# Kernel tuning notes

Measured on AMD Instinct MI355X. Metric: run time of the kernel, lower is better.

Reference implementation:

```python
import jax, jax.numpy as jnp
import numpy as np

B = 16384   # batch
D = 768     # in_features == out_features
H = 768     # expert_hidden_size (must equal D, see MoRALayer wiring)
E = 4       # num_experts_per_level
L = 2       # num_levels
K = 2       # SparseMoE top-k
T = 10      # max_act_steps
LN_EPS = 1e-5


def setup_inputs() -> dict:
    key = jax.random.key(0)
    ks = jax.random.split(key, 8)
    s = 0.02
    return {
        "x": jax.random.normal(ks[0], (B, D), jnp.float32),
        # LSTMCell params (torch gate order i,f,g,o)
        "Wi": jax.random.normal(ks[1], (4 * H, D), jnp.float32) * s,
        "Wh": jax.random.normal(ks[2], (4 * H, H), jnp.float32) * s,
        "bi": jnp.zeros((4 * H,), jnp.float32),
        "bh": jnp.zeros((4 * H,), jnp.float32),
        # halting head
        "Whalt": jax.random.normal(ks[3], (1, H), jnp.float32) * s,
        "bhalt": jnp.zeros((1,), jnp.float32),
        # hierarchical MoE params, stacked over levels (all dims equal: D==H)
        "gateW": jax.random.normal(ks[4], (L, E, H), jnp.float32) * s,
        "gateb": jnp.zeros((L, E), jnp.float32),
        "W1": jax.random.normal(ks[5], (L, E, H, H), jnp.float32) * s,
        "b1": jnp.zeros((L, E, H), jnp.float32),
        "W2": jax.random.normal(ks[6], (L, E, D, H), jnp.float32) * s,
        "b2": jnp.zeros((L, E, D), jnp.float32),
        # LayerNorm
        "gamma": jnp.ones((D,), jnp.float32),
        "beta": jnp.zeros((D,), jnp.float32),
    }


def _act(x, Wi, Wh, bi, bh, Whalt, bhalt):
    """AdaptiveComputationTime: fixed T LSTM steps (faithful worst-case of the
    data-dependent early break). Returns rem * mean_t(h_t) per the torch math:
    avg = sum_t(h_t * rem_final) / n_updates, with rem_final broadcast over t."""
    b = x.shape[0]
    h0 = jnp.zeros((b, H), x.dtype)
    c0 = jnp.zeros((b, H), x.dtype)
    hp0 = jnp.zeros((b, 1), x.dtype)
    rem0 = jnp.zeros((b, 1), x.dtype)
    hsum0 = jnp.zeros((b, H), x.dtype)
    xWi = x @ Wi.T + bi + bh  # constant across steps

    def step(carry, _):
        h, c, hp, rem, hsum = carry
        gates = xWi + h @ Wh.T
        i, f, g, o = jnp.split(gates, 4, axis=-1)
        c = jax.nn.sigmoid(f) * c + jax.nn.sigmoid(i) * jnp.tanh(g)
        h = jax.nn.sigmoid(o) * jnp.tanh(c)
        y = jax.nn.sigmoid(h @ Whalt.T + bhalt)  # [b,1]
        hp = hp + y * (1.0 - hp)
        rem = rem + 1.0 - hp
        return (h, c, hp, rem, hsum + h), None

    (h, c, hp, rem, hsum), _ = jax.lax.scan(
        step, (h0, c0, hp0, rem0, hsum0), None, length=T)
    n_updates = jnp.asarray(float(T), x.dtype)
    avg = rem * hsum / n_updates  # [b,H]
    return avg, hp, n_updates


def _sparse_moe(x, Wg, bg, W1, b1, W2, b2):
    """Top-k expert routing (intended semantics of the torch SparseMoE)."""
    logits = x @ Wg.T + bg                                   # [b,E]
    w, idx = jax.lax.top_k(logits, K)                        # [b,K]
    w = jax.nn.softmax(w, axis=-1)
    hmid = jax.nn.relu(jnp.einsum('bi,ehi->beh', x, W1) + b1)  # [b,E,H]
    eo = jnp.einsum('beh,eoh->beo', hmid, W2) + b2             # [b,E,D]
    sel = jnp.take_along_axis(eo, idx[:, :, None], axis=1)     # [b,K,D]
    return jnp.sum(w[:, :, None] * sel, axis=1)                # [b,D]


def reference(x, Wi, Wh, bi, bh, Whalt, bhalt,
              gateW, gateb, W1, b1, W2, b2, gamma, beta):
    h, _hp, _n = _act(x, Wi, Wh, bi, bh, Whalt, bhalt)
    for l in range(L):
        h = _sparse_moe(h, gateW[l], gateb[l], W1[l], b1[l], W2[l], b2[l])
    mu = jnp.mean(h, axis=-1, keepdims=True)
    var = jnp.mean(jnp.square(h - mu), axis=-1, keepdims=True)
    return (h - mu) * jax.lax.rsqrt(var + LN_EPS) * gamma + beta
```

## Files before the change

### kernel.cpp

```cpp
#include <hip/hip_runtime.h>
#include <cstdint>
#include <cstddef>

#define Bn 16384
#define Dn 768
#define Hn 768
#define G4 3072
#define Tn 10
#define LO_SCALE 4096.0f
#define LO_INV   (1.0f/4096.0f)

typedef _Float16 f16;
typedef _Float16 f16x8 __attribute__((ext_vector_type(8)));
typedef float    f32x4 __attribute__((ext_vector_type(4)));

__device__ __forceinline__ float sigm(float x) { return 1.f / (1.f + expf(-x)); }

__device__ __forceinline__ void gll16(const void* g, void* l) {
    __builtin_amdgcn_global_load_lds((const __attribute__((address_space(1))) void*)g,
                                     (__attribute__((address_space(3))) void*)l, 16, 0, 0);
}

template <bool SPLIT, int EPI, bool BIAS, bool RELU>
__global__ __launch_bounds__(256) void mgemm(
    const f16* __restrict__ Ah, const f16* __restrict__ Al, int lda,
    const f16* __restrict__ Bh, const f16* __restrict__ Bl,
    float* __restrict__ Cf, f16* __restrict__ Ch, f16* __restrict__ Cl, int ldc,
    const float* __restrict__ bias,
    const float* __restrict__ xwi, float* __restrict__ cst, float* __restrict__ hsum,
    f16* __restrict__ hh_out, f16* __restrict__ hl_out,
    long aZ, long bZ, long cZ, long biasZ)
{
    const int z = blockIdx.z;
    if (z) {
        Ah += (long)z * aZ; if (SPLIT) Al += (long)z * aZ;
        Bh += (long)z * bZ; if (SPLIT) Bl += (long)z * bZ;
        if (EPI == 0) Cf += (long)z * cZ;
        if (EPI == 1 || EPI == 2) { Ch += (long)z * cZ; if (EPI == 1) Cl += (long)z * cZ; }
        if (BIAS) bias += (long)z * biasZ;
    }
    __shared__ __align__(16) f16 sA[2][4096];
    __shared__ __align__(16) f16 sB[2][4096];

    const int tid  = threadIdx.x;
    const int w    = tid >> 6, lane = tid & 63;
    const int quad = lane >> 4, l15 = lane & 15;
    const int m0 = blockIdx.x * 128, n0 = blockIdx.y * 128;
    const int wm = (w >> 1) * 64,   wn = (w & 1) * 64;

    f32x4 acc[4][4], accx[4][4];
#pragma unroll
    for (int i = 0; i < 4; i++)
#pragma unroll
        for (int j = 0; j < 4; j++) {
            acc[i][j]  = (f32x4){0.f, 0.f, 0.f, 0.f};
            accx[i][j] = (f32x4){0.f, 0.f, 0.f, 0.f};
        }

    for (int k0 = 0; k0 < 768; k0 += 32) {
        __syncthreads();
#pragma unroll
        for (int u = 0; u < 2; u++) {
            int s = u * 256 + tid;
            int r = s >> 2;
            int c = ((s & 3) - (r >> 1)) & 3;
            gll16(Ah + (long)(m0 + r) * lda + k0 + c * 8, &sA[0][s * 8]);
            gll16(Bh + (long)(n0 + r) * 768 + k0 + c * 8, &sB[0][s * 8]);
            if (SPLIT) {
                gll16(Al + (long)(m0 + r) * lda + k0 + c * 8, &sA[1][s * 8]);
                gll16(Bl + (long)(n0 + r) * 768 + k0 + c * 8, &sB[1][s * 8]);
            }
        }
        __syncthreads();

        f16x8 ah[4], al[4], bh[4], bl[4];
#pragma unroll
        for (int t = 0; t < 4; t++) {
            int ra = wm + t * 16 + l15;
            int ca = (quad + (ra >> 1)) & 3;
            ah[t] = *(const f16x8*)&sA[0][ra * 32 + ca * 8];
            if (SPLIT) al[t] = *(const f16x8*)&sA[1][ra * 32 + ca * 8];
            int rb = wn + t * 16 + l15;
            int cb = (quad + (rb >> 1)) & 3;
            bh[t] = *(const f16x8*)&sB[0][rb * 32 + cb * 8];
            if (SPLIT) bl[t] = *(const f16x8*)&sB[1][rb * 32 + cb * 8];
        }
#pragma unroll
        for (int i = 0; i < 4; i++)
#pragma unroll
            for (int j = 0; j < 4; j++) {
                acc[i][j] = __builtin_amdgcn_mfma_f32_16x16x32_f16(ah[i], bh[j], acc[i][j], 0, 0, 0);
                if (SPLIT) {
                    accx[i][j] = __builtin_amdgcn_mfma_f32_16x16x32_f16(ah[i], bl[j], accx[i][j], 0, 0, 0);
                    accx[i][j] = __builtin_amdgcn_mfma_f32_16x16x32_f16(al[i], bh[j], accx[i][j], 0, 0, 0);
                }
            }
    }

    if (EPI == 3) {
        const int j = ((n0 + wn) >> 2) + l15;
#pragma unroll
        for (int i = 0; i < 4; i++) {
#pragma unroll
            for (int reg = 0; reg < 4; reg++) {
                int r = m0 + wm + i * 16 + quad * 4 + reg;
                long xb = (long)r * G4 + n0 + wn + l15;
                float iv = acc[i][0][reg] + accx[i][0][reg] * LO_INV + xwi[xb];
                float fv = acc[i][1][reg] + accx[i][1][reg] * LO_INV + xwi[xb + 16];
                float gv = acc[i][2][reg] + accx[i][2][reg] * LO_INV + xwi[xb + 32];
                float ov = acc[i][3][reg] + accx[i][3][reg] * LO_INV + xwi[xb + 48];
                long ci = (long)r * Hn + j;
                float cv = sigm(fv) * cst[ci] + sigm(iv) * tanhf(gv);
                float hv = sigm(ov) * tanhf(cv);
                cst[ci] = cv;
                hsum[ci] += hv;
                f16 hh = (f16)hv;
                hh_out[ci] = hh;
                hl_out[ci] = (f16)((hv - (float)hh) * LO_SCALE);
            }
        }
    } else {
#pragma unroll
        for (int i = 0; i < 4; i++)
#pragma unroll
            for (int j = 0; j < 4; j++) {
                int col = n0 + wn + j * 16 + l15;
                float bv = BIAS ? bias[col] : 0.f;
#pragma unroll
                for (int reg = 0; reg < 4; reg++) {
                    int r = m0 + wm + i * 16 + quad * 4 + reg;
                    float v = acc[i][j][reg] + (SPLIT ? accx[i][j][reg] * LO_INV : 0.f) + bv;
                    if (RELU) v = v > 0.f ? v : 0.f;
                    long o = (long)r * ldc + col;
                    if (EPI == 0) Cf[o] = v;
                    else if (EPI == 2) Ch[o] = (f16)v;
                    else {
                        f16 hh = (f16)v;
                        Ch[o] = hh;
                        Cl[o] = (f16)((v - (float)hh) * LO_SCALE);
                    }
                }
            }
    }
}


__global__ void split_plain_k(const float* __restrict__ src, f16* __restrict__ dh,
                              f16* __restrict__ dl, long n) {
    long i = (long)blockIdx.x * 256 + threadIdx.x;
    if (i < n) {
        float v = src[i];
        f16 h = (f16)v;
        dh[i] = h;
        dl[i] = (f16)((v - (float)h) * LO_SCALE);
    }
}

__global__ void split_perm_k(const float* __restrict__ src, f16* __restrict__ dh,
                             f16* __restrict__ dl) {
    int P = blockIdx.x;
    int q = ((P >> 4) & 3) * Hn + (P >> 6) * 16 + (P & 15);
    const float* s = src + (long)q * 768;
    long o = (long)P * 768;
#pragma unroll
    for (int u = 0; u < 3; u++) {
        int kk = threadIdx.x + u * 256;
        float v = s[kk];
        f16 h = (f16)v;
        dh[o + kk] = h;
        dl[o + kk] = (f16)((v - (float)h) * LO_SCALE);
    }
}

__global__ void bsum_perm_k(const float* __restrict__ bi, const float* __restrict__ bh,
                            float* __restrict__ bsum) {
    int P = blockIdx.x * 256 + threadIdx.x;
    if (P < G4) {
        int q = ((P >> 4) & 3) * Hn + (P >> 6) * 16 + (P & 15);
        bsum[P] = bi[q] + bh[q];
    }
}

__global__ __launch_bounds__(256) void lstm0_k(
    const float* __restrict__ xwi, float* __restrict__ cst, float* __restrict__ hsum,
    f16* __restrict__ hh, f16* __restrict__ hl,
    float* __restrict__ hp, float* __restrict__ rem,
    const float* __restrict__ Whalt, const float* __restrict__ bhalt)
{
    const int row = blockIdx.x, tid = threadIdx.x;
    const float* xr = xwi + (long)row * G4;
    const long hb = (long)row * Hn;
    float part = 0.f;
#pragma unroll
    for (int u = 0; u < 3; u++) {
        int j = tid + u * 256;
        int Pb = (j >> 4) * 64 + (j & 15);
        float iv = xr[Pb], fv = xr[Pb + 16], gv = xr[Pb + 32], ov = xr[Pb + 48];
        (void)fv;
        float cv = sigm(iv) * tanhf(gv);
        float hv = sigm(ov) * tanhf(cv);
        cst[hb + j] = cv;
        hsum[hb + j] = hv;
        f16 h = (f16)hv;
        hh[hb + j] = h;
        hl[hb + j] = (f16)((hv - (float)h) * LO_SCALE);
        part += hv * Whalt[j];
    }
    __shared__ float red[256];
    red[tid] = part;
    __syncthreads();
    for (int s = 128; s > 0; s >>= 1) {
        if (tid < s) red[tid] += red[tid + s];
        __syncthreads();
    }
    if (tid == 0) {
        float y = sigm(red[0] + bhalt[0]);
        hp[row] = y;
        rem[row] = 1.f - y;
    }
}

__global__ __launch_bounds__(256) void halt_k(
    const f16* __restrict__ hh, const f16* __restrict__ hl,
    float* __restrict__ hp, float* __restrict__ rem,
    const float* __restrict__ Whalt, const float* __restrict__ bhalt)
{
    const int row = blockIdx.x, tid = threadIdx.x;
    const long hb = (long)row * Hn;
    float part = 0.f;
#pragma unroll
    for (int u = 0; u < 3; u++) {
        int j = tid + u * 256;
        float hv = (float)hh[hb + j] + (float)hl[hb + j] * LO_INV;
        part += hv * Whalt[j];
    }
    __shared__ float red[256];
    red[tid] = part;
    __syncthreads();
    for (int s = 128; s > 0; s >>= 1) {
        if (tid < s) red[tid] += red[tid + s];
        __syncthreads();
    }
    if (tid == 0) {
        float y = sigm(red[0] + bhalt[0]);
        float p = hp[row];
        float np = p + y * (1.f - p);
        hp[row] = np;
        rem[row] += 1.f - np;
    }
}

__global__ void avgsplit_k(const float* __restrict__ hsum, const float* __restrict__ rem,
                           float* __restrict__ xm, f16* __restrict__ xmh, f16* __restrict__ xml) {
    long i = (long)blockIdx.x * 256 + threadIdx.x;
    int row = (int)(i / Hn);
    float v = rem[row] * hsum[i] * (1.f / (float)Tn);
    xm[i] = v;
    f16 h = (f16)v;
    xmh[i] = h;
    xml[i] = (f16)((v - (float)h) * LO_SCALE);
}

__global__ __launch_bounds__(256) void moe_gate_k(
    const float* __restrict__ xm, const float* __restrict__ gW,
    const float* __restrict__ gb, float* __restrict__ wout, int* __restrict__ idxout)
{
    const int row = blockIdx.x, tid = threadIdx.x;
    const float* xr = xm + (long)row * Hn;
    float p[4] = {0.f, 0.f, 0.f, 0.f};
#pragma unroll
    for (int u = 0; u < 3; u++) {
        int j = tid + u * 256;
        float xv = xr[j];
        p[0] += xv * gW[j];
        p[1] += xv * gW[Hn + j];
        p[2] += xv * gW[2 * Hn + j];
        p[3] += xv * gW[3 * Hn + j];
    }
    __shared__ float red[256];
    __shared__ float logit[4];
    for (int e = 0; e < 4; e++) {
        red[tid] = p[e];
        __syncthreads();
        for (int s = 128; s > 0; s >>= 1) {
            if (tid < s) red[tid] += red[tid + s];
            __syncthreads();
        }
        if (tid == 0) logit[e] = red[0] + gb[e];
        __syncthreads();
    }
    if (tid == 0) {
        int i0 = 0;
        for (int e = 1; e < 4; e++) if (logit[e] > logit[i0]) i0 = e;
        int i1 = -1;
        for (int e = 0; e < 4; e++) {
            if (e == i0) continue;
            if (i1 < 0 || logit[e] > logit[i1]) i1 = e;
        }
        float ex = expf(logit[i1] - logit[i0]);
        wout[2 * row] = 1.f / (1.f + ex);
        wout[2 * row + 1] = ex / (1.f + ex);
        idxout[2 * row] = i0;
        idxout[2 * row + 1] = i1;
    }
}

template <bool SO>
__global__ void combine_k(const float* __restrict__ eo, const float* __restrict__ wv,
                          const int* __restrict__ idx, float* __restrict__ dst,
                          f16* __restrict__ dh, f16* __restrict__ dl) {
    long i = (long)blockIdx.x * 256 + threadIdx.x;
    int row = (int)(i / Hn);
    int d = (int)(i - (long)row * Hn);
    long base = (long)row * G4;
    float v = wv[2 * row]     * eo[base + (long)idx[2 * row]     * Hn + d]
            + wv[2 * row + 1] * eo[base + (long)idx[2 * row + 1] * Hn + d];
    dst[i] = v;
    if (SO) {
        f16 h = (f16)v;
        dh[i] = h;
        dl[i] = (f16)((v - (float)h) * LO_SCALE);
    }
}

__global__ __launch_bounds__(256) void layernorm_k(
    const float* __restrict__ in, const float* __restrict__ gamma,
    const float* __restrict__ beta, float* __restrict__ out)
{
    const int row = blockIdx.x, tid = threadIdx.x;
    const float* xr = in + (long)row * Dn;
    float v[3], s = 0.f, s2 = 0.f;
#pragma unroll
    for (int u = 0; u < 3; u++) {
        v[u] = xr[tid + u * 256];
        s += v[u];
        s2 += v[u] * v[u];
    }
    __shared__ float r1[256], r2[256];
    __shared__ float smu, srs;
    r1[tid] = s; r2[tid] = s2;
    __syncthreads();
    for (int st = 128; st > 0; st >>= 1) {
        if (tid < st) { r1[tid] += r1[tid + st]; r2[tid] += r2[tid + st]; }
        __syncthreads();
    }
    if (tid == 0) {
        float mu = r1[0] * (1.f / (float)Dn);
        float var = r2[0] * (1.f / (float)Dn) - mu * mu;
        smu = mu;
        srs = 1.f / sqrtf(var + 1e-5f);
    }
    __syncthreads();
    float mu = smu, rs = srs;
#pragma unroll
    for (int u = 0; u < 3; u++) {
        int j = tid + u * 256;
        out[(long)row * Dn + j] = (v[u] - mu) * rs * gamma[j] + beta[j];
    }
}


extern "C" void kernel_launch(void* const* d_in, const int* in_sizes, int n_in,
                              void* d_out, int out_size, void* d_ws, size_t ws_size,
                              hipStream_t stream) {
    (void)in_sizes; (void)n_in; (void)out_size;
    const float* x     = (const float*)d_in[0];
    const float* Wi    = (const float*)d_in[1];
    const float* Wh    = (const float*)d_in[2];
    const float* bi    = (const float*)d_in[3];
    const float* bh    = (const float*)d_in[4];
    const float* Whalt = (const float*)d_in[5];
    const float* bhalt = (const float*)d_in[6];
    const float* gateW = (const float*)d_in[7];
    const float* gateb = (const float*)d_in[8];
    const float* W1    = (const float*)d_in[9];
    const float* b1    = (const float*)d_in[10];
    const float* W2    = (const float*)d_in[11];
    const float* b2    = (const float*)d_in[12];
    const float* gamma = (const float*)d_in[13];
    const float* beta  = (const float*)d_in[14];
    float* out = (float*)d_out;

    char* p = (char*)d_ws;
    auto carve = [&](size_t bytes) { char* r = p; p += (bytes + 255) & ~(size_t)255; return r; };

    const long WIHN = (long)G4 * 768;
    const long WEHN = (long)8 * 768 * 768;
    f16* Wih = (f16*)carve(WIHN * 2); f16* Wil = (f16*)carve(WIHN * 2);
    f16* Whh = (f16*)carve(WIHN * 2); f16* Whl = (f16*)carve(WIHN * 2);
    f16* W1h = (f16*)carve(WEHN * 2); f16* W1l = (f16*)carve(WEHN * 2);
    f16* W2h = (f16*)carve(WEHN * 2); f16* W2l = (f16*)carve(WEHN * 2);
    float* bsum = (float*)carve(G4 * 4);
    size_t fixed = (size_t)(p - (char*)d_ws);

    int Bc = Bn;
    while (Bc > 128) {
        size_t need = fixed + (size_t)Bc * 46104 + 32 * 256;
        if (need <= ws_size) break;
        Bc >>= 1;
    }
    const int nChunks = Bn / Bc;

    f16*   xh    = (f16*)carve((size_t)Bc * 768 * 2);
    f16*   xl    = (f16*)carve((size_t)Bc * 768 * 2);
    float* xwi   = (float*)carve((size_t)Bc * G4 * 4);
    float* cst   = (float*)carve((size_t)Bc * 768 * 4);
    float* hsumb = (float*)carve((size_t)Bc * 768 * 4);
    float* xm    = (float*)carve((size_t)Bc * 768 * 4);
    f16*   xmh   = (f16*)carve((size_t)Bc * 768 * 2);
    f16*   xml   = (f16*)carve((size_t)Bc * 768 * 2);
    f16*   h0h   = (f16*)carve((size_t)Bc * 768 * 2);
    f16*   h0l   = (f16*)carve((size_t)Bc * 768 * 2);
    f16*   h1h   = (f16*)carve((size_t)Bc * 768 * 2);
    f16*   h1l   = (f16*)carve((size_t)Bc * 768 * 2);
    f16*   hmh   = (f16*)carve((size_t)Bc * G4 * 2);
    f16*   hml   = (f16*)carve((size_t)Bc * G4 * 2);
    float* hp    = (float*)carve((size_t)Bc * 4);
    float* rem   = (float*)carve((size_t)Bc * 4);
    float* wbuf  = (float*)carve((size_t)Bc * 2 * 4);
    int*   ibuf  = (int*)carve((size_t)Bc * 2 * 4);

    split_perm_k<<<G4, 256, 0, stream>>>(Wi, Wih, Wil);
    split_perm_k<<<G4, 256, 0, stream>>>(Wh, Whh, Whl);
    split_plain_k<<<(int)((WEHN + 255) / 256), 256, 0, stream>>>(W1, W1h, W1l, WEHN);
    split_plain_k<<<(int)((WEHN + 255) / 256), 256, 0, stream>>>(W2, W2h, W2l, WEHN);
    bsum_perm_k<<<G4 / 256, 256, 0, stream>>>(bi, bh, bsum);

    dim3 blk(256);
    dim3 g24(Bc / 128, 24, 1);
    dim3 g6z(Bc / 128, 6, 4);
    const int ew = Bc * 3;

    const long EXP_OFF = (long)4 * 768 * 768;

    for (int ch = 0; ch < nChunks; ch++) {
        const float* xc = x + (size_t)ch * Bc * Dn;
        float* outc = out + (size_t)ch * Bc * Dn;

        split_plain_k<<<ew, blk, 0, stream>>>(xc, xh, xl, (long)Bc * 768);

        mgemm<true, 0, true, false><<<g24, blk, 0, stream>>>(
            xh, xl, 768, Wih, Wil, xwi, nullptr, nullptr, G4, bsum,
            nullptr, nullptr, nullptr, nullptr, nullptr, 0, 0, 0, 0);

        lstm0_k<<<Bc, blk, 0, stream>>>(xwi, cst, hsumb, h0h, h0l, hp, rem, Whalt, bhalt);

        for (int t = 1; t < Tn; t++) {
            f16* rah = (t & 1) ? h0h : h1h;
            f16* ral = (t & 1) ? h0l : h1l;
            f16* wah = (t & 1) ? h1h : h0h;
            f16* wal = (t & 1) ? h1l : h0l;
            mgemm<true, 3, false, false><<<g24, blk, 0, stream>>>(
                rah, ral, 768, Whh, Whl, nullptr, nullptr, nullptr, 0, nullptr,
                xwi, cst, hsumb, wah, wal, 0, 0, 0, 0);
            halt_k<<<Bc, blk, 0, stream>>>(wah, wal, hp, rem, Whalt, bhalt);
        }

        avgsplit_k<<<ew, blk, 0, stream>>>(hsumb, rem, xm, xmh, xml);

        float* eo = xwi;
        for (int l = 0; l < 2; l++) {
            moe_gate_k<<<Bc, blk, 0, stream>>>(xm, gateW + (long)l * G4, gateb + l * 4, wbuf, ibuf);
            if (l == 0) {
                mgemm<true, 1, true, true><<<g24, blk, 0, stream>>>(
                    xmh, xml, 768, W1h, W1l, nullptr, hmh, hml, G4, b1,
                    nullptr, nullptr, nullptr, nullptr, nullptr, 0, 0, 0, 0);
                mgemm<true, 0, true, false><<<g6z, blk, 0, stream>>>(
                    hmh, hml, G4, W2h, W2l, eo, nullptr, nullptr, G4, b2,
                    nullptr, nullptr, nullptr, nullptr, nullptr,
                    768, (long)768 * 768, 768, 768);
                combine_k<true><<<ew, blk, 0, stream>>>(eo, wbuf, ibuf, xm, xmh, xml);
            } else {
                mgemm<false, 2, true, true><<<g24, blk, 0, stream>>>(
                    xmh, nullptr, 768, W1h + EXP_OFF, nullptr, nullptr, hmh, nullptr, G4,
                    b1 + G4, nullptr, nullptr, nullptr, nullptr, nullptr, 0, 0, 0, 0);
                mgemm<false, 0, true, false><<<g6z, blk, 0, stream>>>(
                    hmh, nullptr, G4, W2h + EXP_OFF, nullptr, eo, nullptr, nullptr, G4,
                    b2 + G4, nullptr, nullptr, nullptr, nullptr, nullptr,
                    768, (long)768 * 768, 768, 768);
                combine_k<false><<<ew, blk, 0, stream>>>(eo, wbuf, ibuf, hsumb, nullptr, nullptr);
            }
        }

        layernorm_k<<<Bc, blk, 0, stream>>>(hsumb, gamma, beta, outc);
    }
}
```

Measured before the change: 7.327 ms.

## Fuse halting dot into LSTM GEMM epilogue, load B from global, fast math

The per-step halt_k kernel is removed. The halting dot product is computed in the LSTM GEMM epilogue with shuffles and atomicAdd, and a small rem_k kernel reconstructs the remainder from the stored per-step logits. The B operand is now read straight from global memory into registers instead of being staged in LDS, which halves LDS use. sigmoid and tanh switch to exp2/rcp intrinsics. The fp32 copy xm is dropped and workspace buffers are aliased in a shared pool, allowing larger chunks. Risks include atomic contention, reduced accuracy of the fast transcendental functions, and uncoalesced or uncached B loads.

```diff
diff --git a/kernel.cpp b/kernel.cpp
--- a/kernel.cpp
+++ b/kernel.cpp
@@ -14,7 +14,10 @@
 typedef _Float16 f16x8 __attribute__((ext_vector_type(8)));
 typedef float    f32x4 __attribute__((ext_vector_type(4)));
 
-__device__ __forceinline__ float sigm(float x) { return 1.f / (1.f + expf(-x)); }
+__device__ __forceinline__ float fexp2(float x) { return __builtin_amdgcn_exp2f(x); }
+__device__ __forceinline__ float frcp(float x)  { return __builtin_amdgcn_rcpf(x); }
+__device__ __forceinline__ float fsigm(float x) { return frcp(1.f + fexp2(-1.44269504f * x)); }
+__device__ __forceinline__ float ftanh(float x) { return 1.f - 2.f * frcp(1.f + fexp2(2.88539008f * x)); }
 
 __device__ __forceinline__ void gll16(const void* g, void* l) {
     __builtin_amdgcn_global_load_lds((const __attribute__((address_space(1))) void*)g,
@@ -29,6 +32,7 @@
     const float* __restrict__ bias,
     const float* __restrict__ xwi, float* __restrict__ cst, float* __restrict__ hsum,
     f16* __restrict__ hh_out, f16* __restrict__ hl_out,
+    float* __restrict__ dhalt, const float* __restrict__ Whalt,
     long aZ, long bZ, long cZ, long biasZ)
 {
     const int z = blockIdx.z;
@@ -39,8 +43,7 @@
         if (EPI == 1 || EPI == 2) { Ch += (long)z * cZ; if (EPI == 1) Cl += (long)z * cZ; }
         if (BIAS) bias += (long)z * biasZ;
     }
-    __shared__ __align__(16) f16 sA[2][4096];
-    __shared__ __align__(16) f16 sB[2][4096];
+    __shared__ __align__(16) f16 sA[(SPLIT ? 2 : 1) * 4096];
 
     const int tid  = threadIdx.x;
     const int w    = tid >> 6, lane = tid & 63;
@@ -48,13 +51,16 @@
     const int m0 = blockIdx.x * 128, n0 = blockIdx.y * 128;
     const int wm = (w >> 1) * 64,   wn = (w & 1) * 64;
 
+    const f16* Bbase  = Bh + (long)(n0 + wn + l15) * 768 + quad * 8;
+    const f16* Bbasel = SPLIT ? (Bl + (long)(n0 + wn + l15) * 768 + quad * 8) : nullptr;
+
     f32x4 acc[4][4], accx[4][4];
 #pragma unroll
     for (int i = 0; i < 4; i++)
 #pragma unroll
         for (int j = 0; j < 4; j++) {
-            acc[i][j]  = (f32x4){0.f, 0.f, 0.f, 0.f};
-            accx[i][j] = (f32x4){0.f, 0.f, 0.f, 0.f};
+            acc[i][j] = (f32x4){0.f, 0.f, 0.f, 0.f};
+            if (SPLIT) accx[i][j] = (f32x4){0.f, 0.f, 0.f, 0.f};
         }
 
     for (int k0 = 0; k0 < 768; k0 += 32) {
@@ -64,26 +70,25 @@
             int s = u * 256 + tid;
             int r = s >> 2;
             int c = ((s & 3) - (r >> 1)) & 3;
-            gll16(Ah + (long)(m0 + r) * lda + k0 + c * 8, &sA[0][s * 8]);
-            gll16(Bh + (long)(n0 + r) * 768 + k0 + c * 8, &sB[0][s * 8]);
-            if (SPLIT) {
-                gll16(Al + (long)(m0 + r) * lda + k0 + c * 8, &sA[1][s * 8]);
-                gll16(Bl + (long)(n0 + r) * 768 + k0 + c * 8, &sB[1][s * 8]);
-            }
-        }
-        __syncthreads();
-
-        f16x8 ah[4], al[4], bh[4], bl[4];
+            gll16(Ah + (long)(m0 + r) * lda + k0 + c * 8, &sA[s * 8]);
+            if (SPLIT) gll16(Al + (long)(m0 + r) * lda + k0 + c * 8, &sA[4096 + s * 8]);
+        }
+
+        f16x8 bh[4], bl[4];
+#pragma unroll
+        for (int t = 0; t < 4; t++) {
+            bh[t] = *(const f16x8*)(Bbase + (long)t * 12288 + k0);
+            if (SPLIT) bl[t] = *(const f16x8*)(Bbasel + (long)t * 12288 + k0);
+        }
+        __syncthreads();
+
+        f16x8 ah[4], al[4];
 #pragma unroll
         for (int t = 0; t < 4; t++) {
             int ra = wm + t * 16 + l15;
             int ca = (quad + (ra >> 1)) & 3;
-            ah[t] = *(const f16x8*)&sA[0][ra * 32 + ca * 8];
-            if (SPLIT) al[t] = *(const f16x8*)&sA[1][ra * 32 + ca * 8];
-            int rb = wn + t * 16 + l15;
-            int cb = (quad + (rb >> 1)) & 3;
-            bh[t] = *(const f16x8*)&sB[0][rb * 32 + cb * 8];
-            if (SPLIT) bl[t] = *(const f16x8*)&sB[1][rb * 32 + cb * 8];
+            ah[t] = *(const f16x8*)&sA[ra * 32 + ca * 8];
+            if (SPLIT) al[t] = *(const f16x8*)&sA[4096 + ra * 32 + ca * 8];
         }
 #pragma unroll
         for (int i = 0; i < 4; i++)
@@ -99,6 +104,7 @@
 
     if (EPI == 3) {
         const int j = ((n0 + wn) >> 2) + l15;
+        const float wj = Whalt[j];
 #pragma unroll
         for (int i = 0; i < 4; i++) {
 #pragma unroll
@@ -110,13 +116,19 @@
                 float gv = acc[i][2][reg] + accx[i][2][reg] * LO_INV + xwi[xb + 32];
                 float ov = acc[i][3][reg] + accx[i][3][reg] * LO_INV + xwi[xb + 48];
                 long ci = (long)r * Hn + j;
-                float cv = sigm(fv) * cst[ci] + sigm(iv) * tanhf(gv);
-                float hv = sigm(ov) * tanhf(cv);
+                float cv = fsigm(fv) * cst[ci] + fsigm(iv) * ftanh(gv);
+                float hv = fsigm(ov) * ftanh(cv);
                 cst[ci] = cv;
                 hsum[ci] += hv;
                 f16 hh = (f16)hv;
                 hh_out[ci] = hh;
                 hl_out[ci] = (f16)((hv - (float)hh) * LO_SCALE);
+                float p = hv * wj;
+                p += __shfl_xor(p, 1, 16);
+                p += __shfl_xor(p, 2, 16);
+                p += __shfl_xor(p, 4, 16);
+                p += __shfl_xor(p, 8, 16);
+                if (l15 == 0) atomicAdd(&dhalt[r], p);
             }
         }
     } else {
@@ -183,9 +195,8 @@
 
 __global__ __launch_bounds__(256) void lstm0_k(
     const float* __restrict__ xwi, float* __restrict__ cst, float* __restrict__ hsum,
-    f16* __restrict__ hh, f16* __restrict__ hl,
-    float* __restrict__ hp, float* __restrict__ rem,
-    const float* __restrict__ Whalt, const float* __restrict__ bhalt)
+    f16* __restrict__ hh, f16* __restrict__ hl, float* __restrict__ d0,
+    const float* __restrict__ Whalt)
 {
     const int row = blockIdx.x, tid = threadIdx.x;
     const float* xr = xwi + (long)row * G4;
@@ -195,10 +206,9 @@
     for (int u = 0; u < 3; u++) {
         int j = tid + u * 256;
         int Pb = (j >> 4) * 64 + (j & 15);
-        float iv = xr[Pb], fv = xr[Pb + 16], gv = xr[Pb + 32], ov = xr[Pb + 48];
-        (void)fv;
-        float cv = sigm(iv) * tanhf(gv);
-        float hv = sigm(ov) * tanhf(cv);
+        float iv = xr[Pb], gv = xr[Pb + 32], ov = xr[Pb + 48];
+        float cv = fsigm(iv) * ftanh(gv);
+        float hv = fsigm(ov) * ftanh(cv);
         cst[hb + j] = cv;
         hsum[hb + j] = hv;
         f16 h = (f16)hv;
@@ -213,65 +223,46 @@
         if (tid < s) red[tid] += red[tid + s];
         __syncthreads();
     }
-    if (tid == 0) {
-        float y = sigm(red[0] + bhalt[0]);
-        hp[row] = y;
-        rem[row] = 1.f - y;
-    }
-}
-
-__global__ __launch_bounds__(256) void halt_k(
-    const f16* __restrict__ hh, const f16* __restrict__ hl,
-    float* __restrict__ hp, float* __restrict__ rem,
-    const float* __restrict__ Whalt, const float* __restrict__ bhalt)
-{
-    const int row = blockIdx.x, tid = threadIdx.x;
-    const long hb = (long)row * Hn;
-    float part = 0.f;
-#pragma unroll
-    for (int u = 0; u < 3; u++) {
-        int j = tid + u * 256;
-        float hv = (float)hh[hb + j] + (float)hl[hb + j] * LO_INV;
-        part += hv * Whalt[j];
-    }
-    __shared__ float red[256];
-    red[tid] = part;
-    __syncthreads();
-    for (int s = 128; s > 0; s >>= 1) {
-        if (tid < s) red[tid] += red[tid + s];
-        __syncthreads();
-    }
-    if (tid == 0) {
-        float y = sigm(red[0] + bhalt[0]);
-        float p = hp[row];
-        float np = p + y * (1.f - p);
-        hp[row] = np;
-        rem[row] += 1.f - np;
-    }
+    if (tid == 0) d0[row] = red[0];
+}
+
+__global__ void rem_k(const float* __restrict__ d, const float* __restrict__ bhalt,
+                      float* __restrict__ rem, int bc) {
+    int r = blockIdx.x * 256 + threadIdx.x;
+    if (r >= bc) return;
+    float b0 = bhalt[0];
+    float prod = 1.f, rm = 0.f;
+#pragma unroll
+    for (int t = 0; t < Tn; t++) {
+        float y = fsigm(d[(long)t * bc + r] + b0);
+        prod *= (1.f - y);
+        rm += prod;
+    }
+    rem[r] = rm;
 }
 
 __global__ void avgsplit_k(const float* __restrict__ hsum, const float* __restrict__ rem,
-                           float* __restrict__ xm, f16* __restrict__ xmh, f16* __restrict__ xml) {
+                           f16* __restrict__ xmh, f16* __restrict__ xml) {
     long i = (long)blockIdx.x * 256 + threadIdx.x;
     int row = (int)(i / Hn);
     float v = rem[row] * hsum[i] * (1.f / (float)Tn);
-    xm[i] = v;
     f16 h = (f16)v;
     xmh[i] = h;
     xml[i] = (f16)((v - (float)h) * LO_SCALE);
 }
 
 __global__ __launch_bounds__(256) void moe_gate_k(
-    const float* __restrict__ xm, const float* __restrict__ gW,
-    const float* __restrict__ gb, float* __restrict__ wout, int* __restrict__ idxout)
+    const f16* __restrict__ xmh, const f16* __restrict__ xml,
+    const float* __restrict__ gW, const float* __restrict__ gb,
+    float* __restrict__ wout, int* __restrict__ idxout)
 {
     const int row = blockIdx.x, tid = threadIdx.x;
-    const float* xr = xm + (long)row * Hn;
+    const long xb = (long)row * Hn;
     float p[4] = {0.f, 0.f, 0.f, 0.f};
 #pragma unroll
     for (int u = 0; u < 3; u++) {
         int j = tid + u * 256;
-        float xv = xr[j];
+        float xv = (float)xmh[xb + j] + (float)xml[xb + j] * LO_INV;
         p[0] += xv * gW[j];
         p[1] += xv * gW[Hn + j];
         p[2] += xv * gW[2 * Hn + j];
@@ -315,11 +306,12 @@
     long base = (long)row * G4;
     float v = wv[2 * row]     * eo[base + (long)idx[2 * row]     * Hn + d]
             + wv[2 * row + 1] * eo[base + (long)idx[2 * row + 1] * Hn + d];
-    dst[i] = v;
     if (SO) {
         f16 h = (f16)v;
         dh[i] = h;
         dl[i] = (f16)((v - (float)h) * LO_SCALE);
+    } else {
+        dst[i] = v;
     }
 }
 
@@ -395,30 +387,31 @@
 
     int Bc = Bn;
     while (Bc > 128) {
-        size_t need = fixed + (size_t)Bc * 46104 + 32 * 256;
+        size_t need = fixed + (size_t)Bc * 34100 + 64 * 256;
         if (need <= ws_size) break;
         Bc >>= 1;
     }
     const int nChunks = Bn / Bc;
 
-    f16*   xh    = (f16*)carve((size_t)Bc * 768 * 2);
-    f16*   xl    = (f16*)carve((size_t)Bc * 768 * 2);
     float* xwi   = (float*)carve((size_t)Bc * G4 * 4);
     float* cst   = (float*)carve((size_t)Bc * 768 * 4);
     float* hsumb = (float*)carve((size_t)Bc * 768 * 4);
-    float* xm    = (float*)carve((size_t)Bc * 768 * 4);
-    f16*   xmh   = (f16*)carve((size_t)Bc * 768 * 2);
-    f16*   xml   = (f16*)carve((size_t)Bc * 768 * 2);
-    f16*   h0h   = (f16*)carve((size_t)Bc * 768 * 2);
-    f16*   h0l   = (f16*)carve((size_t)Bc * 768 * 2);
-    f16*   h1h   = (f16*)carve((size_t)Bc * 768 * 2);
-    f16*   h1l   = (f16*)carve((size_t)Bc * 768 * 2);
-    f16*   hmh   = (f16*)carve((size_t)Bc * G4 * 2);
-    f16*   hml   = (f16*)carve((size_t)Bc * G4 * 2);
-    float* hp    = (float*)carve((size_t)Bc * 4);
+    char*  pool  = carve((size_t)Bc * 15360);
+    float* d     = (float*)carve((size_t)Bc * Tn * 4);
     float* rem   = (float*)carve((size_t)Bc * 4);
     float* wbuf  = (float*)carve((size_t)Bc * 2 * 4);
     int*   ibuf  = (int*)carve((size_t)Bc * 2 * 4);
+
+    f16* xh  = (f16*)pool;
+    f16* xl  = xh + (size_t)Bc * 768;
+    f16* h0h = xl + (size_t)Bc * 768;
+    f16* h0l = h0h + (size_t)Bc * 768;
+    f16* h1h = h0l + (size_t)Bc * 768;
+    f16* h1l = h1h + (size_t)Bc * 768;
+    f16* xmh = (f16*)pool;
+    f16* xml = xmh + (size_t)Bc * 768;
+    f16* hmh = xml + (size_t)Bc * 768;
+    f16* hml = hmh + (size_t)Bc * G4;
 
     split_perm_k<<<G4, 256, 0, stream>>>(Wi, Wih, Wil);
     split_perm_k<<<G4, 256, 0, stream>>>(Wh, Whh, Whl);
@@ -430,7 +423,6 @@
     dim3 g24(Bc / 128, 24, 1);
     dim3 g6z(Bc / 128, 6, 4);
     const int ew = Bc * 3;
-
     const long EXP_OFF = (long)4 * 768 * 768;
 
     for (int ch = 0; ch < nChunks; ch++) {
@@ -441,9 +433,10 @@
 
         mgemm<true, 0, true, false><<<g24, blk, 0, stream>>>(
             xh, xl, 768, Wih, Wil, xwi, nullptr, nullptr, G4, bsum,
-            nullptr, nullptr, nullptr, nullptr, nullptr, 0, 0, 0, 0);
-
-        lstm0_k<<<Bc, blk, 0, stream>>>(xwi, cst, hsumb, h0h, h0l, hp, rem, Whalt, bhalt);
+            nullptr, nullptr, nullptr, nullptr, nullptr, nullptr, nullptr, 0, 0, 0, 0);
+
+        hipMemsetAsync(d, 0, (size_t)Bc * Tn * 4, stream);
+        lstm0_k<<<Bc, blk, 0, stream>>>(xwi, cst, hsumb, h0h, h0l, d, Whalt);
 
         for (int t = 1; t < Tn; t++) {
             f16* rah = (t & 1) ? h0h : h1h;
@@ -452,31 +445,33 @@
             f16* wal = (t & 1) ? h1l : h0l;
             mgemm<true, 3, false, false><<<g24, blk, 0, stream>>>(
                 rah, ral, 768, Whh, Whl, nullptr, nullptr, nullptr, 0, nullptr,
-                xwi, cst, hsumb, wah, wal, 0, 0, 0, 0);
-            halt_k<<<Bc, blk, 0, stream>>>(wah, wal, hp, rem, Whalt, bhalt);
-        }
-
-        avgsplit_k<<<ew, blk, 0, stream>>>(hsumb, rem, xm, xmh, xml);
+                xwi, cst, hsumb, wah, wal, d + (size_t)t * Bc, Whalt, 0, 0, 0, 0);
+        }
+
+        rem_k<<<(Bc + 255) / 256, blk, 0, stream>>>(d, bhalt, rem, Bc);
+        avgsplit_k<<<ew, blk, 0, stream>>>(hsumb, rem, xmh, xml);
 
         float* eo = xwi;
         for (int l = 0; l < 2; l++) {
-            moe_gate_k<<<Bc, blk, 0, stream>>>(xm, gateW + (long)l * G4, gateb + l * 4, wbuf, ibuf);
+            moe_gate_k<<<Bc, blk, 0, stream>>>(xmh, xml, gateW + (long)l * G4,
+                                               gateb + l * 4, wbuf, ibuf);
             if (l == 0) {
                 mgemm<true, 1, true, true><<<g24, blk, 0, stream>>>(
                     xmh, xml, 768, W1h, W1l, nullptr, hmh, hml, G4, b1,
-                    nullptr, nullptr, nullptr, nullptr, nullptr, 0, 0, 0, 0);
+                    nullptr, nullptr, nullptr, nullptr, nullptr, nullptr, nullptr, 0, 0, 0, 0);
                 mgemm<true, 0, true, false><<<g6z, blk, 0, stream>>>(
                     hmh, hml, G4, W2h, W2l, eo, nullptr, nullptr, G4, b2,
-                    nullptr, nullptr, nullptr, nullptr, nullptr,
+                    nullptr, nullptr, nullptr, nullptr, nullptr, nullptr, nullptr,
                     768, (long)768 * 768, 768, 768);
-                combine_k<true><<<ew, blk, 0, stream>>>(eo, wbuf, ibuf, xm, xmh, xml);
+                combine_k<true><<<ew, blk, 0, stream>>>(eo, wbuf, ibuf, nullptr, xmh, xml);
             } else {
                 mgemm<false, 2, true, true><<<g24, blk, 0, stream>>>(
                     xmh, nullptr, 768, W1h + EXP_OFF, nullptr, nullptr, hmh, nullptr, G4,
-                    b1 + G4, nullptr, nullptr, nullptr, nullptr, nullptr, 0, 0, 0, 0);
+                    b1 + G4, nullptr, nullptr, nullptr, nullptr, nullptr, nullptr, nullptr,
+                    0, 0, 0, 0);
                 mgemm<false, 0, true, false><<<g6z, blk, 0, stream>>>(
                     hmh, nullptr, G4, W2h + EXP_OFF, nullptr, eo, nullptr, nullptr, G4,
-                    b2 + G4, nullptr, nullptr, nullptr, nullptr, nullptr,
+                    b2 + G4, nullptr, nullptr, nullptr, nullptr, nullptr, nullptr, nullptr,
                     768, (long)768 * 768, 768, 768);
                 combine_k<false><<<ew, blk, 0, stream>>>(eo, wbuf, ibuf, hsumb, nullptr, nullptr);
             }
```

Result: slower. 8.509 ms (+16.1%).
